# Kernel optimization log

Hardware: AMD Instinct MI355X
Metric: run time of the kernel (lower is better)

Reference implementation:

```python
import jax, jax.numpy as jnp
import numpy as np

EPS = 1e-5
NUM_HEADS = 16


def layernorm(x, g, b):
    m = jnp.mean(x, axis=-1, keepdims=True)
    v = jnp.mean(jnp.square(x - m), axis=-1, keepdims=True)
    return (x - m) * jax.lax.rsqrt(v + EPS) * g + b


def setup_inputs() -> dict:
    key = jax.random.key(0)
    ks = jax.random.split(key, 8)
    B, S, E, F = 16, 512, 1024, 4096
    s_e = 1.0 / np.sqrt(E)
    s_f = 1.0 / np.sqrt(F)
    return {
        "input": jax.random.normal(ks[0], (B, S, E), jnp.float32),
        "ln1_g": jnp.ones((E,), jnp.float32),
        "ln1_b": jnp.zeros((E,), jnp.float32),
        "wq": jax.random.normal(ks[1], (E, E), jnp.float32) * s_e,
        "bq": jnp.zeros((E,), jnp.float32),
        "wk": jax.random.normal(ks[2], (E, E), jnp.float32) * s_e,
        "bk": jnp.zeros((E,), jnp.float32),
        "wv": jax.random.normal(ks[3], (E, E), jnp.float32) * s_e,
        "bv": jnp.zeros((E,), jnp.float32),
        "wo": jax.random.normal(ks[4], (E, E), jnp.float32) * s_e,
        "bo": jnp.zeros((E,), jnp.float32),
        "ln2_g": jnp.ones((E,), jnp.float32),
        "ln2_b": jnp.zeros((E,), jnp.float32),
        "w1": jax.random.normal(ks[5], (E, F), jnp.float32) * s_e,
        "b1": jnp.zeros((F,), jnp.float32),
        "w2": jax.random.normal(ks[6], (F, E), jnp.float32) * s_f,
        "b2": jnp.zeros((E,), jnp.float32),
    }


def attention(x, wq, bq, wk, bk, wv, bv, wo, bo):
    B, S, E = x.shape
    H = NUM_HEADS
    D = E // H
    q = (x @ wq + bq).reshape(B, S, H, D)
    k = (x @ wk + bk).reshape(B, S, H, D)
    v = (x @ wv + bv).reshape(B, S, H, D)
    scores = jnp.einsum("bqhd,bkhd->bhqk", q, k) * (1.0 / np.sqrt(D))
    attn = jax.nn.softmax(scores, axis=-1)
    out = jnp.einsum("bhqk,bkhd->bqhd", attn, v).reshape(B, S, E)
    return out @ wo + bo


def reference(input, ln1_g, ln1_b, wq, bq, wk, bk, wv, bv, wo, bo,
              ln2_g, ln2_b, w1, b1, w2, b2):
    # pre-LN attention + residual
    x = layernorm(input, ln1_g, ln1_b)
    x = attention(x, wq, bq, wk, bk, wv, bv, wo, bo)
    x = x + input
    # pre-LN MLP (GELU exact, matching nn.GELU default) + residual
    y = layernorm(x, ln2_g, ln2_b)
    y = jax.nn.gelu(y @ w1 + b1, approximate=False)
    y = y @ w2 + b2
    return x + y
```

## Files before the change

kernel.cpp:

```cpp
#include <hip/hip_runtime.h>
#include <hip/hip_bf16.h>


typedef __bf16 bf16x8 __attribute__((ext_vector_type(8)));
typedef __bf16 bf16x4 __attribute__((ext_vector_type(4)));
typedef float  f32x4  __attribute__((ext_vector_type(4)));

#define EPI_QKV  0
#define EPI_RES  1
#define EPI_GELU 2
#define EPI_V    3

__device__ __forceinline__ void async_copy16(const void* g, void* l) {
  __builtin_amdgcn_global_load_lds((const __attribute__((address_space(1))) void*)g,
                                   (__attribute__((address_space(3))) void*)l, 16, 0, 0);
}

__device__ __forceinline__ float block_sum(float v, float* red) {
#pragma unroll
  for (int off = 32; off; off >>= 1) v += __shfl_down(v, off);
  const int w = threadIdx.x >> 6;
  __syncthreads();
  if ((threadIdx.x & 63) == 0) red[w] = v;
  __syncthreads();
  return red[0] + red[1] + red[2] + red[3];
}

__device__ __forceinline__ void ln_row(const float* __restrict__ x,
                                       const float* __restrict__ g,
                                       const float* __restrict__ bta,
                                       __bf16* __restrict__ out, int row,
                                       float* red) {
  const int t = threadIdx.x;
  const float4 v = ((const float4*)(x + (size_t)row * 1024))[t];
  float s = v.x + v.y + v.z + v.w;
  s = block_sum(s, red);
  const float mean = s * (1.0f / 1024.0f);
  const float d0 = v.x - mean, d1 = v.y - mean, d2 = v.z - mean, d3 = v.w - mean;
  float vs = d0 * d0 + d1 * d1 + d2 * d2 + d3 * d3;
  vs = block_sum(vs, red);
  const float rstd = rsqrtf(vs * (1.0f / 1024.0f) + 1e-5f);
  const float4 gg = ((const float4*)g)[t];
  const float4 bb = ((const float4*)bta)[t];
  bf16x4 o;
  o[0] = (__bf16)(d0 * rstd * gg.x + bb.x);
  o[1] = (__bf16)(d1 * rstd * gg.y + bb.y);
  o[2] = (__bf16)(d2 * rstd * gg.z + bb.z);
  o[3] = (__bf16)(d3 * rstd * gg.w + bb.w);
  ((bf16x4*)out)[(size_t)row * 256 + t] = o;
}

__global__ __launch_bounds__(256) void ln_kernel(const float* __restrict__ x,
                                                 const float* __restrict__ g,
                                                 const float* __restrict__ bta,
                                                 __bf16* __restrict__ out) {
  __shared__ float red[8];
  ln_row(x, g, bta, out, blockIdx.x, red);
}

__global__ __launch_bounds__(256) void prep_ln(
    const float* __restrict__ wq, const float* __restrict__ wk,
    const float* __restrict__ wv, const float* __restrict__ wo,
    const float* __restrict__ w1, const float* __restrict__ w2,
    const float* __restrict__ bq, const float* __restrict__ bk,
    const float* __restrict__ bv,
    __bf16* __restrict__ wqkvT, __bf16* __restrict__ woT,
    __bf16* __restrict__ w1T, __bf16* __restrict__ w2T, float* __restrict__ bqkv,
    const float* __restrict__ input, const float* __restrict__ ln1_g,
    const float* __restrict__ ln1_b, __bf16* __restrict__ lnout) {
  const int bid = blockIdx.x;
  if (bid >= 12300) {
    __shared__ float red[8];
    ln_row(input, ln1_g, ln1_b, lnout, bid - 12300, red);
    return;
  }
  if (bid >= 12288) {
    const int i = (bid - 12288) * 256 + threadIdx.x;
    bqkv[i] = (i < 1024) ? bq[i] : ((i < 2048) ? bk[i - 1024] : bv[i - 2048]);
    return;
  }
  const float* in;
  __bf16* out;
  int K, N, tile;
  if (bid < 4096) {
    const int w = bid >> 10;
    tile = bid & 1023;
    in = (w == 0) ? wq : (w == 1) ? wk : (w == 2) ? wv : wo;
    out = (w == 3) ? woT : (wqkvT + (size_t)w * 1024 * 1024);
    K = 1024; N = 1024;
  } else if (bid < 8192) { tile = bid - 4096; in = w1; out = w1T; K = 1024; N = 4096; }
  else                   { tile = bid - 8192; in = w2; out = w2T; K = 4096; N = 1024; }
  const int ntx = N >> 5;
  const int bx = tile % ntx, by = tile / ntx;
  const int n0 = bx * 32, k0 = by * 32;

  __shared__ float tilebuf[32][33];
  const int tx = threadIdx.x & 31, ty = threadIdx.x >> 5;
#pragma unroll
  for (int i = 0; i < 4; i++)
    tilebuf[ty + i * 8][tx] = in[(size_t)(k0 + ty + i * 8) * N + n0 + tx];
  __syncthreads();
#pragma unroll
  for (int i = 0; i < 4; i++)
    out[(size_t)(n0 + ty + i * 8) * K + k0 + tx] = (__bf16)tilebuf[tx][ty + i * 8];
}

template <int EPI>
__global__ __launch_bounds__(256, 2) void gemm_bt(const __bf16* __restrict__ A,
                                                  const __bf16* __restrict__ Bt,
                                                  const float* __restrict__ bias,
                                                  const float* __restrict__ res,
                                                  void* __restrict__ out,
                                                  void* __restrict__ out2,
                                                  int N, int K) {
  __shared__ __bf16 lA[128 * 64];
  __shared__ __bf16 lB[128 * 64];
  const int t = threadIdx.x;
  const int wave = t >> 6, lane = t & 63;
  const int lm = lane & 15, lq = lane >> 4;

  const int Ntiles = gridDim.x;
  const int flat = blockIdx.y * Ntiles + blockIdx.x;
  const int xcd = flat & 7;
  const int local = flat >> 3;
  const int tn = local % Ntiles;
  const int tm = (local / Ntiles) * 8 + xcd;
  const int m0 = tm * 128, n0 = tn * 128;
  const int wm = (wave & 1) * 64, wn = (wave >> 1) * 64;

  f32x4 acc[4][4] = {};

  const int srow = t >> 3, sslot = t & 7;
  const int schunk = sslot ^ (srow & 7);
  const __bf16* aSrc = A + (size_t)(m0 + srow) * K + schunk * 8;
  const __bf16* bSrc = Bt + (size_t)(n0 + srow) * K + schunk * 8;

  for (int k0 = 0; k0 < K; k0 += 64) {
#pragma unroll
    for (int i = 0; i < 4; i++) {
      async_copy16(aSrc + (size_t)(i * 32) * K, lA + i * 2048 + t * 8);
      async_copy16(bSrc + (size_t)(i * 32) * K, lB + i * 2048 + t * 8);
    }
    aSrc += 64; bSrc += 64;
    __syncthreads();
#pragma unroll
    for (int kk = 0; kk < 2; kk++) {
      bf16x8 af[4], bf[4];
      const int slot = (kk * 4 + lq) ^ (lm & 7);
#pragma unroll
      for (int i = 0; i < 4; i++) {
        af[i] = *(const bf16x8*)&lA[(wm + i * 16 + lm) * 64 + slot * 8];
        bf[i] = *(const bf16x8*)&lB[(wn + i * 16 + lm) * 64 + slot * 8];
      }
#pragma unroll
      for (int mi = 0; mi < 4; mi++)
#pragma unroll
        for (int ni = 0; ni < 4; ni++)
          acc[mi][ni] = __builtin_amdgcn_mfma_f32_16x16x32_bf16(af[mi], bf[ni], acc[mi][ni], 0, 0, 0);
    }
    __syncthreads();
  }

#pragma unroll
  for (int mi = 0; mi < 4; mi++) {
    const int gr = m0 + wm + mi * 16 + lq * 4;
#pragma unroll
    for (int ni = 0; ni < 4; ni++) {
      const int gc = n0 + wn + ni * 16 + lm;
      const float bv = bias[gc];
#pragma unroll
      for (int r = 0; r < 4; r++) {
        float v = acc[mi][ni][r] + bv;
        const int row = gr + r;
        if (EPI == EPI_GELU) {
          v = 0.5f * v * (1.0f + erff(v * 0.70710678118654752f));
          ((__bf16*)out)[(size_t)row * N + gc] = (__bf16)v;
        } else if (EPI == EPI_RES) {
          ((float*)out)[(size_t)row * N + gc] = v + res[(size_t)row * N + gc];
        } else if (EPI == EPI_V) {
          const int d = gc & 63, hh = gc >> 6;
          const int bb = row >> 9, ss = row & 511;
          ((__bf16*)out2)[(((size_t)bb * 16 + hh) * 64 + d) * 512 + ss] = (__bf16)v;
        } else {
          if (gc < 2048) {
            ((__bf16*)out)[(size_t)row * 2048 + gc] = (__bf16)v;
          } else {
            const int d = gc & 63, hh = (gc - 2048) >> 6;
            const int bb = row >> 9, ss = row & 511;
            ((__bf16*)out2)[(((size_t)bb * 16 + hh) * 64 + d) * 512 + ss] = (__bf16)v;
          }
        }
      }
    }
  }
}

#define MFMA_QUAD(MI0)                                                         \
  do {                                                                         \
    _Pragma("unroll") for (int kk = 0; kk < 2; ++kk) {                         \
      _Pragma("unroll") for (int ni = 0; ni < 4; ++ni) {                       \
        acc[MI0][ni] = __builtin_amdgcn_mfma_f32_16x16x32_bf16(                \
            af[MI0][kk], bf[ni][kk], acc[MI0][ni], 0, 0, 0);                   \
        acc[(MI0) + 1][ni] = __builtin_amdgcn_mfma_f32_16x16x32_bf16(          \
            af[(MI0) + 1][kk], bf[ni][kk], acc[(MI0) + 1][ni], 0, 0, 0);       \
      }                                                                        \
    }                                                                          \
  } while (0)

#define READ_A8(MI)                                                            \
  _Pragma("unroll") for (int kk = 0; kk < 2; ++kk)                             \
      af[MI][kk] = *(const bf16x8*)&bufA[(wm * 128 + (MI)*16 + lm) * 64 +      \
                                         (((kk * 4 + lq) ^ sw) * 8)];

template <int EPI>
__global__ __launch_bounds__(512, 2) void gemm8_bt(const __bf16* __restrict__ A,
                                                   const __bf16* __restrict__ Bt,
                                                   const float* __restrict__ bias,
                                                   void* __restrict__ out,
                                                   void* __restrict__ out2,
                                                   int N, int K) {
  __shared__ __bf16 lA[2 * 256 * 64];
  __shared__ __bf16 lB[2 * 256 * 64];
  const int t = threadIdx.x;
  const int wave = t >> 6, lane = t & 63;
  const int lm = lane & 15, lq = lane >> 4, sw = lm & 7;
  const int wm = wave >> 2, wn = wave & 3;

  const int Ntiles = gridDim.x;
  const int flat = blockIdx.y * Ntiles + blockIdx.x;
  const int xcd = flat & 7;
  const int local = flat >> 3;
  const int tn = local % Ntiles;
  const int tm = (local / Ntiles) * 8 + xcd;
  const int m0 = tm * 256, n0 = tn * 256;

  const int NT = K >> 6;

  const int srow = t >> 3;
  const int schunk = (t & 7) ^ (srow & 7);
  const __bf16* aBase = A + (size_t)(m0 + srow) * K + schunk * 8;
  const __bf16* bBase = Bt + (size_t)(n0 + srow) * K + schunk * 8;
  __bf16* ldA = lA + t * 8;
  __bf16* ldB = lB + t * 8;

  auto stage = [&](int h) {
    if (h >= 4 * NT) return;
    const int tau = h >> 2, type = h & 3, hf = type & 1;
    const size_t roff = (size_t)(hf * 128) * K + (size_t)tau * 64;
    const int loff = (tau & 1) * 16384 + hf * 8192;
    if (type < 2) {
      async_copy16(aBase + roff, ldA + loff);
      async_copy16(aBase + roff + (size_t)64 * K, ldA + loff + 4096);
    } else {
      async_copy16(bBase + roff, ldB + loff);
      async_copy16(bBase + roff + (size_t)64 * K, ldB + loff + 4096);
    }
  };

  f32x4 acc[8][4] = {};

  for (int h = 0; h < 6; ++h) stage(h);
  asm volatile("s_waitcnt vmcnt(4)" ::: "memory");
  __builtin_amdgcn_s_barrier();

  for (int tt = 0; tt < NT; ++tt) {
    const __bf16* bufA = lA + (tt & 1) * 16384;
    const __bf16* bufB = lB + (tt & 1) * 16384;
    bf16x8 af[8][2], bf[4][2];

#pragma unroll
    for (int ni = 0; ni < 4; ++ni)
#pragma unroll
      for (int kk = 0; kk < 2; ++kk)
        bf[ni][kk] = *(const bf16x8*)&bufB[(wn * 64 + ni * 16 + lm) * 64 +
                                           (((kk * 4 + lq) ^ sw) * 8)];
    READ_A8(0)
    READ_A8(1)
    READ_A8(2)
    READ_A8(3)
    stage(4 * tt + 6);
    stage(4 * tt + 7);
    __builtin_amdgcn_s_barrier();
    asm volatile("s_waitcnt lgkmcnt(0)" ::: "memory");
    __builtin_amdgcn_sched_barrier(0);
    __builtin_amdgcn_s_setprio(1);
    MFMA_QUAD(0);
    MFMA_QUAD(2);
    __builtin_amdgcn_s_setprio(0);
    __builtin_amdgcn_s_barrier();

    READ_A8(4)
    READ_A8(5)
    READ_A8(6)
    READ_A8(7)
    __builtin_amdgcn_s_barrier();
    asm volatile("s_waitcnt lgkmcnt(0)" ::: "memory");
    __builtin_amdgcn_sched_barrier(0);
    __builtin_amdgcn_s_setprio(1);
    MFMA_QUAD(4);
    MFMA_QUAD(6);
    __builtin_amdgcn_s_setprio(0);
    __builtin_amdgcn_s_barrier();

    if (tt < NT - 1) {
      stage(4 * tt + 8);
      stage(4 * tt + 9);
      if (tt == NT - 2) asm volatile("s_waitcnt vmcnt(0)" ::: "memory");
      else              asm volatile("s_waitcnt vmcnt(4)" ::: "memory");
      __builtin_amdgcn_s_barrier();
    }
  }

#pragma unroll
  for (int mi = 0; mi < 8; ++mi) {
    const int gr = m0 + wm * 128 + mi * 16 + lq * 4;
#pragma unroll
    for (int ni = 0; ni < 4; ++ni) {
      const int gc = n0 + wn * 64 + ni * 16 + lm;
      const float bv = bias[gc];
#pragma unroll
      for (int r = 0; r < 4; ++r) {
        float v = acc[mi][ni][r] + bv;
        const int row = gr + r;
        if (EPI == EPI_GELU) {
          v = 0.5f * v * (1.0f + erff(v * 0.70710678118654752f));
          ((__bf16*)out)[(size_t)row * N + gc] = (__bf16)v;
        } else {
          if (gc < 2048) {
            ((__bf16*)out)[(size_t)row * 2048 + gc] = (__bf16)v;
          } else {
            const int d = gc & 63, hh = (gc - 2048) >> 6;
            const int bb = row >> 9, ss = row & 511;
            ((__bf16*)out2)[(((size_t)bb * 16 + hh) * 64 + d) * 512 + ss] = (__bf16)v;
          }
        }
      }
    }
  }
}

__global__ __launch_bounds__(256, 2) void attn_kernel(const __bf16* __restrict__ qk,
                                                      const __bf16* __restrict__ Vt,
                                                      __bf16* __restrict__ outA) {
  __shared__ __bf16 lK[2][128 * 64];
  __shared__ __bf16 lV[2][64 * 128];
  __shared__ __bf16 lP[4][16 * 128];
  const int t = threadIdx.x, wave = t >> 6, lane = t & 63;
  const int lm = lane & 15, lq = lane >> 4;
  const int sw = lm & 7;
  const int flat = blockIdx.x;
  const int xcd = flat & 7, local = flat >> 3;
  const int qt = local & 1;
  const int bh = xcd * 32 + (local >> 1);
  const int h = bh & 15, b = bh >> 4;
  const int qbase = qt * 256 + wave * 64;

  bf16x8 aq[4][2];
#pragma unroll
  for (int qg = 0; qg < 4; qg++) {
    const size_t qrow = (size_t)(b * 512 + qbase + qg * 16 + lm) * 2048 + h * 64;
    aq[qg][0] = *(const bf16x8*)&qk[qrow + lq * 8];
    aq[qg][1] = *(const bf16x8*)&qk[qrow + 32 + lq * 8];
  }

  float mrow[4][4], lrow[4][4];
  f32x4 o[4][4] = {};
#pragma unroll
  for (int qg = 0; qg < 4; qg++)
#pragma unroll
    for (int r = 0; r < 4; r++) { mrow[qg][r] = -3e38f; lrow[qg][r] = 0.f; }

  const int krow = t >> 3;
  const int kchunk = (t & 7) ^ (krow & 7);
  const __bf16* kSrc = qk + (size_t)(b * 512 + krow) * 2048 + 1024 + h * 64 + kchunk * 8;
  const int vrow = t >> 4;
  const int vchunk = (t & 15) ^ (vrow & 7);
  const __bf16* vSrc = Vt + ((size_t)bh * 64 + vrow) * 512 + vchunk * 8;

  auto stage = [&](int kt) {
    __bf16* dK = &lK[kt & 1][t * 8];
    __bf16* dV = &lV[kt & 1][t * 8];
#pragma unroll
    for (int i = 0; i < 4; i++) {
      async_copy16(kSrc + (size_t)(kt * 128 + i * 32) * 2048, dK + i * 2048);
      async_copy16(vSrc + kt * 128 + (size_t)(i * 16) * 512, dV + i * 2048);
    }
  };

  stage(0);
  for (int kt = 0; kt < 4; kt++) {
    if (kt < 3) {
      stage(kt + 1);
      asm volatile("s_waitcnt vmcnt(8)" ::: "memory");
    } else {
      asm volatile("s_waitcnt vmcnt(0)" ::: "memory");
    }
    __builtin_amdgcn_s_barrier();
    const __bf16* bK = lK[kt & 1];
    const __bf16* bV = lV[kt & 1];

#pragma unroll
    for (int qg = 0; qg < 4; qg++) {
      f32x4 s[8];
      __builtin_amdgcn_s_setprio(1);
#pragma unroll
      for (int ni = 0; ni < 8; ni++) {
        bf16x8 bk0 = *(const bf16x8*)&bK[(ni * 16 + lm) * 64 + ((lq ^ sw) * 8)];
        bf16x8 bk1 = *(const bf16x8*)&bK[(ni * 16 + lm) * 64 + (((4 + lq) ^ sw) * 8)];
        f32x4 z = {};
        z = __builtin_amdgcn_mfma_f32_16x16x32_bf16(aq[qg][0], bk0, z, 0, 0, 0);
        z = __builtin_amdgcn_mfma_f32_16x16x32_bf16(aq[qg][1], bk1, z, 0, 0, 0);
        s[ni] = z;
      }
      __builtin_amdgcn_s_setprio(0);
#pragma unroll
      for (int ni = 0; ni < 8; ni++)
#pragma unroll
        for (int r = 0; r < 4; r++) s[ni][r] *= 0.125f;

      float mnew[4], alpha[4];
#pragma unroll
      for (int r = 0; r < 4; r++) {
        float mx = s[0][r];
#pragma unroll
        for (int ni = 1; ni < 8; ni++) mx = fmaxf(mx, s[ni][r]);
#pragma unroll
        for (int off = 1; off < 16; off <<= 1) mx = fmaxf(mx, __shfl_xor(mx, off));
        mnew[r] = fmaxf(mrow[qg][r], mx);
        alpha[r] = __expf(mrow[qg][r] - mnew[r]);
        mrow[qg][r] = mnew[r];
      }
      float rs[4] = {0.f, 0.f, 0.f, 0.f};
#pragma unroll
      for (int ni = 0; ni < 8; ni++)
#pragma unroll
        for (int r = 0; r < 4; r++) {
          const float p = __expf(s[ni][r] - mnew[r]);
          s[ni][r] = p;
          rs[r] += p;
        }
#pragma unroll
      for (int r = 0; r < 4; r++) {
#pragma unroll
        for (int off = 1; off < 16; off <<= 1) rs[r] += __shfl_xor(rs[r], off);
        lrow[qg][r] = lrow[qg][r] * alpha[r] + rs[r];
      }

#pragma unroll
      for (int ni = 0; ni < 8; ni++) {
        const int chunk = ni * 2 + (lm >> 3);
#pragma unroll
        for (int r = 0; r < 4; r++) {
          const int q = lq * 4 + r;
          lP[wave][q * 128 + ((chunk ^ (q & 7)) * 8) + (lm & 7)] = (__bf16)s[ni][r];
        }
      }
      asm volatile("s_waitcnt lgkmcnt(0)" ::: "memory");
      bf16x8 ap[4];
#pragma unroll
      for (int kc = 0; kc < 4; kc++)
        ap[kc] = *(const bf16x8*)&lP[wave][lm * 128 + (((kc * 4 + lq) ^ sw) * 8)];

#pragma unroll
      for (int di = 0; di < 4; di++)
#pragma unroll
        for (int r = 0; r < 4; r++) o[qg][di][r] *= alpha[r];

      __builtin_amdgcn_s_setprio(1);
#pragma unroll
      for (int di = 0; di < 4; di++) {
#pragma unroll
        for (int kc = 0; kc < 4; kc++) {
          bf16x8 bv = *(const bf16x8*)&bV[(di * 16 + lm) * 128 + (((kc * 4 + lq) ^ sw) * 8)];
          o[qg][di] = __builtin_amdgcn_mfma_f32_16x16x32_bf16(ap[kc], bv, o[qg][di], 0, 0, 0);
        }
      }
      __builtin_amdgcn_s_setprio(0);
    }
    __builtin_amdgcn_s_barrier();
  }

#pragma unroll
  for (int qg = 0; qg < 4; qg++)
#pragma unroll
    for (int di = 0; di < 4; di++)
#pragma unroll
      for (int r = 0; r < 4; r++) {
        const float v = o[qg][di][r] / lrow[qg][r];
        outA[(size_t)(b * 512 + qbase + qg * 16 + lq * 4 + r) * 1024 + h * 64 + di * 16 + lm] = (__bf16)v;
      }
}

extern "C" void kernel_launch(void* const* d_in, const int* in_sizes, int n_in,
                              void* d_out, int out_size, void* d_ws, size_t ws_size,
                              hipStream_t stream) {
  const float* input = (const float*)d_in[0];
  const float* ln1_g = (const float*)d_in[1];
  const float* ln1_b = (const float*)d_in[2];
  const float* wq = (const float*)d_in[3];
  const float* bq = (const float*)d_in[4];
  const float* wk = (const float*)d_in[5];
  const float* bk = (const float*)d_in[6];
  const float* wv = (const float*)d_in[7];
  const float* bv = (const float*)d_in[8];
  const float* wo = (const float*)d_in[9];
  const float* bo = (const float*)d_in[10];
  const float* ln2_g = (const float*)d_in[11];
  const float* ln2_b = (const float*)d_in[12];
  const float* w1 = (const float*)d_in[13];
  const float* b1 = (const float*)d_in[14];
  const float* w2 = (const float*)d_in[15];
  const float* b2 = (const float*)d_in[16];

  char* ws = (char*)d_ws;
  __bf16* wqkvT = (__bf16*)(ws + 0);
  __bf16* woT   = (__bf16*)(ws + ((size_t)6 << 20));
  __bf16* w1T   = (__bf16*)(ws + ((size_t)8 << 20));
  __bf16* w2T   = (__bf16*)(ws + ((size_t)16 << 20));
  __bf16* qkbuf = (__bf16*)(ws + ((size_t)24 << 20));
  __bf16* vtbuf = (__bf16*)(ws + ((size_t)56 << 20));
  __bf16* abuf  = (__bf16*)(ws + ((size_t)72 << 20));
  float*  xbuf  = (float*) (ws + ((size_t)24 << 20));
  __bf16* ylnbuf= (__bf16*)(ws + ((size_t)56 << 20));
  __bf16* hbuf  = (__bf16*)(ws + ((size_t)72 << 20));
  float*  bqkv  = (float*) (ws + ((size_t)136 << 20));

  const dim3 blk(256);
  const dim3 blk8(512);
  prep_ln<<<20492, blk, 0, stream>>>(wq, wk, wv, wo, w1, w2, bq, bk, bv,
                                     wqkvT, woT, w1T, w2T, bqkv,
                                     input, ln1_g, ln1_b, abuf);
  gemm8_bt<EPI_QKV><<<dim3(8, 32), blk8, 0, stream>>>(abuf, wqkvT, bqkv,
                                                      qkbuf, vtbuf, 2048, 1024);
  gemm_bt<EPI_V><<<dim3(8, 64), blk, 0, stream>>>(abuf, wqkvT + (size_t)2048 * 1024,
                                                  bqkv + 2048, nullptr,
                                                  nullptr, vtbuf, 1024, 1024);
  attn_kernel<<<512, blk, 0, stream>>>(qkbuf, vtbuf, abuf);
  gemm_bt<EPI_RES><<<dim3(8, 64), blk, 0, stream>>>(abuf, woT, bo, input,
                                                    xbuf, nullptr, 1024, 1024);
  ln_kernel<<<8192, blk, 0, stream>>>(xbuf, ln2_g, ln2_b, ylnbuf);
  gemm8_bt<EPI_GELU><<<dim3(16, 32), blk8, 0, stream>>>(ylnbuf, w1T, b1,
                                                        hbuf, nullptr, 4096, 1024);
  gemm_bt<EPI_RES><<<dim3(8, 64), blk, 0, stream>>>(hbuf, w2T, b2, xbuf,
                                                    d_out, nullptr, 1024, 4096);
}
```

Before: 478.7 us.

## Transpose QK^T MFMA operands so each lane owns one query row in softmax

Swaps the A/B operands of the score MFMA so the S tile comes out transposed, giving each lane a single query row (lm) with its 4 accumulator values along the key axis. Row max and row sum then need only two cross-lane shuffles instead of four per register, and mrow/lrow shrink to one scalar per query group. P is written to LDS as packed 4-element vectors with a new swizzle rather than scalar bf16 stores. The cost is extra __shfl calls to redistribute alpha and the final denominator back to the O-accumulator layout, plus a new LDS swizzle that may carry bank conflicts.

```diff
diff --git a/kernel.cpp b/kernel.cpp
--- a/kernel.cpp
+++ b/kernel.cpp
@@ -363,12 +363,10 @@
     aq[qg][1] = *(const bf16x8*)&qk[qrow + 32 + lq * 8];
   }
 
-  float mrow[4][4], lrow[4][4];
+  float mrow[4], lrow[4];
   f32x4 o[4][4] = {};
 #pragma unroll
-  for (int qg = 0; qg < 4; qg++)
-#pragma unroll
-    for (int r = 0; r < 4; r++) { mrow[qg][r] = -3e38f; lrow[qg][r] = 0.f; }
+  for (int qg = 0; qg < 4; qg++) { mrow[qg] = -3e38f; lrow[qg] = 0.f; }
 
   const int krow = t >> 3;
   const int kchunk = (t & 7) ^ (krow & 7);
@@ -408,8 +406,8 @@
         bf16x8 bk0 = *(const bf16x8*)&bK[(ni * 16 + lm) * 64 + ((lq ^ sw) * 8)];
         bf16x8 bk1 = *(const bf16x8*)&bK[(ni * 16 + lm) * 64 + (((4 + lq) ^ sw) * 8)];
         f32x4 z = {};
-        z = __builtin_amdgcn_mfma_f32_16x16x32_bf16(aq[qg][0], bk0, z, 0, 0, 0);
-        z = __builtin_amdgcn_mfma_f32_16x16x32_bf16(aq[qg][1], bk1, z, 0, 0, 0);
+        z = __builtin_amdgcn_mfma_f32_16x16x32_bf16(bk0, aq[qg][0], z, 0, 0, 0);
+        z = __builtin_amdgcn_mfma_f32_16x16x32_bf16(bk1, aq[qg][1], z, 0, 0, 0);
         s[ni] = z;
       }
       __builtin_amdgcn_s_setprio(0);
@@ -418,53 +416,52 @@
 #pragma unroll
         for (int r = 0; r < 4; r++) s[ni][r] *= 0.125f;
 
-      float mnew[4], alpha[4];
-#pragma unroll
-      for (int r = 0; r < 4; r++) {
-        float mx = s[0][r];
-#pragma unroll
-        for (int ni = 1; ni < 8; ni++) mx = fmaxf(mx, s[ni][r]);
-#pragma unroll
-        for (int off = 1; off < 16; off <<= 1) mx = fmaxf(mx, __shfl_xor(mx, off));
-        mnew[r] = fmaxf(mrow[qg][r], mx);
-        alpha[r] = __expf(mrow[qg][r] - mnew[r]);
-        mrow[qg][r] = mnew[r];
-      }
-      float rs[4] = {0.f, 0.f, 0.f, 0.f};
+      float tmax[8];
 #pragma unroll
       for (int ni = 0; ni < 8; ni++)
+        tmax[ni] = fmaxf(fmaxf(s[ni][0], s[ni][1]), fmaxf(s[ni][2], s[ni][3]));
+      float mx = fmaxf(fmaxf(fmaxf(tmax[0], tmax[1]), fmaxf(tmax[2], tmax[3])),
+                       fmaxf(fmaxf(tmax[4], tmax[5]), fmaxf(tmax[6], tmax[7])));
+      mx = fmaxf(mx, __shfl_xor(mx, 16));
+      mx = fmaxf(mx, __shfl_xor(mx, 32));
+      const float mnew = fmaxf(mrow[qg], mx);
+      const float alpha = __expf(mrow[qg] - mnew);
+      mrow[qg] = mnew;
+      float rs = 0.f;
+#pragma unroll
+      for (int ni = 0; ni < 8; ni++)
 #pragma unroll
         for (int r = 0; r < 4; r++) {
-          const float p = __expf(s[ni][r] - mnew[r]);
+          const float p = __expf(s[ni][r] - mnew);
           s[ni][r] = p;
-          rs[r] += p;
+          rs += p;
         }
-#pragma unroll
-      for (int r = 0; r < 4; r++) {
-#pragma unroll
-        for (int off = 1; off < 16; off <<= 1) rs[r] += __shfl_xor(rs[r], off);
-        lrow[qg][r] = lrow[qg][r] * alpha[r] + rs[r];
-      }
+      rs += __shfl_xor(rs, 16);
+      rs += __shfl_xor(rs, 32);
+      lrow[qg] = lrow[qg] * alpha + rs;
 
 #pragma unroll
       for (int ni = 0; ni < 8; ni++) {
-        const int chunk = ni * 2 + (lm >> 3);
-#pragma unroll
-        for (int r = 0; r < 4; r++) {
-          const int q = lq * 4 + r;
-          lP[wave][q * 128 + ((chunk ^ (q & 7)) * 8) + (lm & 7)] = (__bf16)s[ni][r];
-        }
+        bf16x4 pw;
+        pw[0] = (__bf16)s[ni][0];
+        pw[1] = (__bf16)s[ni][1];
+        pw[2] = (__bf16)s[ni][2];
+        pw[3] = (__bf16)s[ni][3];
+        *(bf16x4*)&lP[wave][lm * 128 + (((4 * ni + lq) ^ (lm & 6)) * 4)] = pw;
       }
       asm volatile("s_waitcnt lgkmcnt(0)" ::: "memory");
       bf16x8 ap[4];
 #pragma unroll
       for (int kc = 0; kc < 4; kc++)
-        ap[kc] = *(const bf16x8*)&lP[wave][lm * 128 + (((kc * 4 + lq) ^ sw) * 8)];
-
+        ap[kc] = *(const bf16x8*)&lP[wave][lm * 128 + (((8 * kc + 2 * lq) ^ (lm & 6)) * 4)];
+
+      float alr[4];
+#pragma unroll
+      for (int r = 0; r < 4; r++) alr[r] = __shfl(alpha, lq * 4 + r);
 #pragma unroll
       for (int di = 0; di < 4; di++)
 #pragma unroll
-        for (int r = 0; r < 4; r++) o[qg][di][r] *= alpha[r];
+        for (int r = 0; r < 4; r++) o[qg][di][r] *= alr[r];
 
       __builtin_amdgcn_s_setprio(1);
 #pragma unroll
@@ -481,14 +478,18 @@
   }
 
 #pragma unroll
-  for (int qg = 0; qg < 4; qg++)
+  for (int qg = 0; qg < 4; qg++) {
+    float lrq[4];
+#pragma unroll
+    for (int r = 0; r < 4; r++) lrq[r] = __shfl(lrow[qg], lq * 4 + r);
 #pragma unroll
     for (int di = 0; di < 4; di++)
 #pragma unroll
       for (int r = 0; r < 4; r++) {
-        const float v = o[qg][di][r] / lrow[qg][r];
+        const float v = o[qg][di][r] / lrq[r];
         outA[(size_t)(b * 512 + qbase + qg * 16 + lq * 4 + r) * 1024 + h * 64 + di * 16 + lm] = (__bf16)v;
       }
+  }
 }
 
 extern "C" void kernel_launch(void* const* d_in, const int* in_sizes, int n_in,
```

Result: slower. 546.2 us (median of 2 runs) (+14.1%).
